# Performance work log

Hardware: AMD Instinct MI355X
Metric: run time of the kernel (lower is better)

The kernel has to match this reference:

```python
import jax, jax.numpy as jnp
import numpy as np

N_HEADS = 16
EPS = 1e-6

def _feature_map(x):
    return jax.nn.elu(x) + 1.0

def setup_inputs() -> dict:
    key = jax.random.key(0)
    k1, k2, k3 = jax.random.split(key, 3)
    B, S, D = 1, 2048, 1024
    x = jax.random.normal(k1, (B, S, D), dtype=jnp.float32)
    causal_mask = jnp.tril(jnp.ones((S, S), dtype=bool))[None, None]  # (1,1,S,S)
    # scale weights like nn.Linear default init (roughly 1/sqrt(fan_in))
    W_qkv = jax.random.normal(k2, (D, 3 * D), dtype=jnp.float32) / np.sqrt(D)
    W_out = jax.random.normal(k3, (D, D), dtype=jnp.float32) / np.sqrt(D)
    return {"x": x, "causal_mask": causal_mask, "W_qkv": W_qkv, "W_out": W_out}

def reference(x, causal_mask, W_qkv, W_out):
    B, S, D = x.shape
    H = N_HEADS
    hd = D // H
    qkv = x @ W_qkv                              # (B,S,3D)
    q, k, v = jnp.split(qkv, 3, axis=-1)
    def to_heads(t):
        return t.reshape(B, S, H, hd).transpose(0, 2, 1, 3)  # (B,H,S,hd)
    q, k, v = to_heads(q), to_heads(k), to_heads(v)
    phi_q = _feature_map(q)
    phi_k = _feature_map(k)
    k_cum = jnp.cumsum(phi_k, axis=2)                        # (B,H,S,hd)
    kv = jnp.einsum('bhsi,bhsj->bhsij', phi_k, v)            # (B,H,S,hd,hd)
    kv_cum = jnp.cumsum(kv, axis=2)
    numer = jnp.einsum('bhsi,bhsij->bhsj', phi_q, kv_cum)    # (B,H,S,hd)
    denom = jnp.einsum('bhsi,bhsi->bhs', phi_q, k_cum) + EPS
    attn_out = numer / denom[..., None]
    attn_out = attn_out.transpose(0, 2, 1, 3).reshape(B, S, D)
    return attn_out @ W_out
```

## Files before the change

kernel.cpp:

```cpp
#include <hip/hip_runtime.h>
#include <cstddef>
#include <cstdint>

#define SEQ 2048
#define DIM 1024
#define NH 16
#define HD 64
#define CK 64
#define NCK (SEQ / CK)
#define KVR 65
#define KVRP 80

typedef __attribute__((ext_vector_type(8))) short short8;
typedef __attribute__((ext_vector_type(8))) unsigned short ushort8;
typedef __attribute__((ext_vector_type(4))) float fx4;

__device__ __forceinline__ float phi_fn(float x) {
    return x > 0.f ? x + 1.f : __expf(x);
}
__device__ __forceinline__ float bf2f(unsigned short u) {
    return __uint_as_float((unsigned int)u << 16);
}
__device__ __forceinline__ unsigned short f2bf(float f) {
    unsigned int u = __float_as_uint(f);
    unsigned int r = (u + 0x7FFFu + ((u >> 16) & 1u)) >> 16;
    return (unsigned short)r;
}

__device__ __forceinline__ short8 lds_read_frag(const unsigned short* base, int row, int kcol) {
    int byte = row * 128 + kcol * 2; byte ^= (row & 7) << 4;
    return *(const short8*)((const char*)base + byte);
}

__device__ __forceinline__ int swz_t(int row, int col) {
    int byte = row * 128 + col * 2;
    return byte ^ ((((row & 7) ^ ((row >> 3) & 7))) << 4);
}
__device__ __forceinline__ void lds_write16_t(unsigned short* base, int row, int col, short8 v) {
    *(short8*)((char*)base + swz_t(row, col)) = v;
}
__device__ __forceinline__ void lds_write2_t(unsigned short* base, int row, int col, unsigned short v) {
    *(unsigned short*)((char*)base + swz_t(row, col)) = v;
}
__device__ __forceinline__ short8 lds_read_frag_t(const unsigned short* base, int row, int kcol) {
    return *(const short8*)((const char*)base + swz_t(row, kcol));
}

template<int N> __device__ __forceinline__ void waitv() {
    if constexpr (N == 0)       asm volatile("s_waitcnt vmcnt(0)"  ::: "memory");
    else if constexpr (N == 4)  asm volatile("s_waitcnt vmcnt(4)"  ::: "memory");
    else if constexpr (N == 5)  asm volatile("s_waitcnt vmcnt(5)"  ::: "memory");
    else if constexpr (N == 6)  asm volatile("s_waitcnt vmcnt(6)"  ::: "memory");
    else if constexpr (N == 8)  asm volatile("s_waitcnt vmcnt(8)"  ::: "memory");
    else if constexpr (N == 10) asm volatile("s_waitcnt vmcnt(10)" ::: "memory");
    else if constexpr (N == 12) asm volatile("s_waitcnt vmcnt(12)" ::: "memory");
    else                        asm volatile("s_waitcnt vmcnt(0)"  ::: "memory");
}

__global__ __launch_bounds__(256)
void prep_fused(const float* __restrict__ x, unsigned short* __restrict__ xb,
                const float* __restrict__ W1, unsigned short* __restrict__ WT1,
                const float* __restrict__ W2, unsigned short* __restrict__ WT2)
{
    __shared__ float t[32][33];
    int b = blockIdx.x;
    if (b < 2048) {
        const int i = (b * 256 + threadIdx.x) * 4;
        float4 v = *(const float4*)&x[i];
        ushort4 o;
        o.x = f2bf(v.x); o.y = f2bf(v.y); o.z = f2bf(v.z); o.w = f2bf(v.w);
        *(ushort4*)&xb[i] = o;
        return;
    }
    b -= 2048;
    const float* W; unsigned short* WT; int N, kb, nb;
    if (b < 96 * 32) {
        W = W1; WT = WT1; N = 3 * DIM;
        nb = (b % 96) * 32; kb = (b / 96) * 32;
    } else {
        b -= 96 * 32;
        W = W2; WT = WT2; N = DIM;
        nb = (b % 32) * 32; kb = (b / 32) * 32;
    }
    const int c = threadIdx.x & 31, r0 = threadIdx.x >> 5;
    #pragma unroll
    for (int i = 0; i < 4; ++i) {
        const int r = r0 + i * 8;
        t[r][c] = W[(size_t)(kb + r) * N + nb + c];
    }
    __syncthreads();
    #pragma unroll
    for (int i = 0; i < 4; ++i) {
        const int r = r0 + i * 8;
        WT[(size_t)(nb + r) * DIM + kb + c] = f2bf(t[c][r]);
    }
}

template<int WAVES_M, int WAVES_N, int NFRAG, int OUT_BF16>
__global__ __launch_bounds__(WAVES_M * WAVES_N * 64)
void gemm_pipe(const unsigned short* __restrict__ A,
               const unsigned short* __restrict__ BT,
               void* __restrict__ Cout, int M, int N, int K)
{
    constexpr int BN      = WAVES_N * NFRAG * 16;
    constexpr int THREADS = WAVES_M * WAVES_N * 64;
    constexpr int CHUNK   = THREADS * 16;
    constexpr int ALOADS  = (128 * 64 * 2) / CHUNK;
    constexpr int BLOADS  = (BN * 64 * 2) / CHUNK;
    constexpr int LOADS   = ALOADS + BLOADS;

    __shared__ unsigned short As[3][128 * 64];
    __shared__ unsigned short Bs[3][BN * 64];

    const int tid = threadIdx.x, lane = tid & 63, wave = tid >> 6;
    const int wm = (wave / WAVES_N) * 64;
    const int wn = (wave % WAVES_N) * (NFRAG * 16);

    int wg = blockIdx.y * gridDim.x + blockIdx.x;
    const int cpx = (gridDim.x * gridDim.y) >> 3;
    wg = (wg & 7) * cpx + (wg >> 3);
    const int bx = wg / gridDim.y;
    const int by = wg % gridDim.y;

    const int m0 = by * 128, n0 = bx * BN;
    const unsigned short* Abase = A + (size_t)m0 * K;
    const unsigned short* Bbase = BT + (size_t)n0 * K;
    const int nt = K >> 6;
    const int fr = lane & 15, fk = (lane >> 4) * 8;

    fx4 acc[4][NFRAG] = {};

    auto STAGE = [&](int slot, int t) {
        const int k0 = t << 6;
        #pragma unroll
        for (int q = 0; q < ALOADS; ++q) {
            const int L = q * CHUNK + tid * 16;
            const int row = L >> 7;
            const int srcb = L ^ ((row & 7) << 4);
            const unsigned short* g = Abase + (size_t)row * K + k0 + ((srcb & 127) >> 1);
            __builtin_amdgcn_global_load_lds(
                (const __attribute__((address_space(1))) void*)g,
                (__attribute__((address_space(3))) void*)((char*)&As[slot][0] + q * CHUNK + wave * 1024),
                16, 0, 0);
        }
        #pragma unroll
        for (int q = 0; q < BLOADS; ++q) {
            const int L = q * CHUNK + tid * 16;
            const int row = L >> 7;
            const int srcb = L ^ ((row & 7) << 4);
            const unsigned short* g = Bbase + (size_t)row * K + k0 + ((srcb & 127) >> 1);
            __builtin_amdgcn_global_load_lds(
                (const __attribute__((address_space(1))) void*)g,
                (__attribute__((address_space(3))) void*)((char*)&Bs[slot][0] + q * CHUNK + wave * 1024),
                16, 0, 0);
        }
    };

    STAGE(0, 0); STAGE(1, 1);
    waitv<LOADS>();
    __builtin_amdgcn_s_barrier();

    for (int t = 0; t < nt; ++t) {
        const int cur = t % 3;
        short8 a0[4], a1[4], b0[NFRAG], b1[NFRAG];
        #pragma unroll
        for (int i = 0; i < 4; ++i) {
            a0[i] = lds_read_frag(&As[cur][0], wm + i * 16 + fr, fk);
            a1[i] = lds_read_frag(&As[cur][0], wm + i * 16 + fr, 32 + fk);
        }
        #pragma unroll
        for (int j = 0; j < NFRAG; ++j) {
            b0[j] = lds_read_frag(&Bs[cur][0], wn + j * 16 + fr, fk);
            b1[j] = lds_read_frag(&Bs[cur][0], wn + j * 16 + fr, 32 + fk);
        }

        const bool pf = (t + 2 < nt);
        if (pf) STAGE((t + 2) % 3, t + 2);

        __builtin_amdgcn_s_setprio(1);
        #pragma unroll
        for (int i = 0; i < 4; ++i)
            #pragma unroll
            for (int j = 0; j < NFRAG; ++j)
                acc[i][j] = __builtin_amdgcn_mfma_f32_16x16x32_bf16(a0[i], b0[j], acc[i][j], 0, 0, 0);
        #pragma unroll
        for (int i = 0; i < 4; ++i)
            #pragma unroll
            for (int j = 0; j < NFRAG; ++j)
                acc[i][j] = __builtin_amdgcn_mfma_f32_16x16x32_bf16(a1[i], b1[j], acc[i][j], 0, 0, 0);
        __builtin_amdgcn_s_setprio(0);

        if (pf) waitv<LOADS>(); else waitv<0>();
        __builtin_amdgcn_s_barrier();
    }

    const int cr = (lane >> 4) * 4, cc = lane & 15;
    #pragma unroll
    for (int i = 0; i < 4; ++i)
        #pragma unroll
        for (int j = 0; j < NFRAG; ++j) {
            const int m = m0 + wm + i * 16 + cr;
            const int n = n0 + wn + j * 16 + cc;
            #pragma unroll
            for (int r = 0; r < 4; ++r) {
                const float v = acc[i][j][r];
                if (OUT_BF16)
                    ((unsigned short*)Cout)[(size_t)(m + r) * N + n] = f2bf(v);
                else
                    ((float*)Cout)[(size_t)(m + r) * N + n] = v;
            }
        }
}

__global__ __launch_bounds__(256)
void chunk_kv(const unsigned short* __restrict__ qkv, float* __restrict__ kvs)
{
    const int c = blockIdx.x, h = blockIdx.y;
    __shared__ unsigned short kT[64 * 64];
    __shared__ unsigned short vT[KVRP * 64];
    const int tid = threadIdx.x, lane = tid & 63, wave = tid >> 6;
    const int s0 = c * CK;

    #pragma unroll
    for (int part = 0; part < 2; ++part) {
        const int s = (tid >> 3) + part * 32;
        const int d0 = (tid & 7) * 8;
        const size_t base = (size_t)(s0 + s) * (3 * DIM) + (size_t)h * HD + d0;
        ushort8 kk = *(const ushort8*)&qkv[base + DIM];
        ushort8 vv = *(const ushort8*)&qkv[base + 2 * DIM];
        #pragma unroll
        for (int u = 0; u < 8; ++u) {
            lds_write2_t(kT, d0 + u, s, f2bf(phi_fn(bf2f(kk[u]))));
            lds_write2_t(vT, d0 + u, s, vv[u]);
        }
    }
    if (tid < 64) lds_write2_t(vT, 64, tid, 0x3F80);
    for (int idx = tid; idx < 15 * 64; idx += 256)
        lds_write2_t(vT, 65 + (idx >> 6), idx & 63, 0);
    __syncthreads();

    fx4 acc[5] = {};
    #pragma unroll
    for (int ks = 0; ks < 2; ++ks) {
        short8 b = lds_read_frag_t(kT, wave * 16 + (lane & 15), ks * 32 + (lane >> 4) * 8);
        #pragma unroll
        for (int mt = 0; mt < 5; ++mt) {
            short8 a = lds_read_frag_t(vT, mt * 16 + (lane & 15), ks * 32 + (lane >> 4) * 8);
            acc[mt] = __builtin_amdgcn_mfma_f32_16x16x32_bf16(a, b, acc[mt], 0, 0, 0);
        }
    }
    float* dst = kvs + (size_t)(h * NCK + c) * KVR * 64;
    const int i = wave * 16 + (lane & 15);
    #pragma unroll
    for (int mt = 0; mt < 5; ++mt)
        #pragma unroll
        for (int t = 0; t < 4; ++t) {
            const int j = mt * 16 + (lane >> 4) * 4 + t;
            if (j < KVR) dst[(size_t)j * 64 + i] = acc[mt][t];
        }
}

__global__ __launch_bounds__(256)
void scan_kv(const float* __restrict__ kvs, unsigned short* __restrict__ kvpb)
{
    const int e = blockIdx.x * 256 + threadIdx.x;
    if (e >= NH * KVR * 64) return;
    const int h = e / (KVR * 64), off = e % (KVR * 64);
    const float* src = kvs + (size_t)h * NCK * KVR * 64 + off;
    unsigned short* dst = kvpb + (size_t)h * NCK * KVR * 64 + off;
    float v[NCK];
    #pragma unroll
    for (int c2 = 0; c2 < NCK; ++c2) v[c2] = src[(size_t)c2 * KVR * 64];
    float run = 0.f;
    #pragma unroll
    for (int c2 = 0; c2 < NCK; ++c2) {
        dst[(size_t)c2 * KVR * 64] = f2bf(run);
        run += v[c2];
    }
}

__global__ __launch_bounds__(256)
void attn_chunk(const unsigned short* __restrict__ qkv,
                const unsigned short* __restrict__ kvpb,
                unsigned short* __restrict__ attnb)
{
    const int c = blockIdx.x, h = blockIdx.y;
    __shared__ unsigned short q_s[64 * 64];
    __shared__ unsigned short k_s[64 * 64];
    __shared__ unsigned short p_s[64 * 64];
    __shared__ unsigned short vT[KVRP * 64];
    __shared__ unsigned short kvp[KVRP * 64];
    const int tid = threadIdx.x, lane = tid & 63, wave = tid >> 6;
    const int s0 = c * CK;

    #pragma unroll
    for (int part = 0; part < 2; ++part) {
        const int s = (tid >> 3) + part * 32;
        const int d0 = (tid & 7) * 8;
        const size_t base = (size_t)(s0 + s) * (3 * DIM) + (size_t)h * HD + d0;
        ushort8 qq = *(const ushort8*)&qkv[base];
        ushort8 kk = *(const ushort8*)&qkv[base + DIM];
        ushort8 vv = *(const ushort8*)&qkv[base + 2 * DIM];
        short8 qo, ko;
        #pragma unroll
        for (int u = 0; u < 8; ++u) {
            qo[u] = (short)f2bf(phi_fn(bf2f(qq[u])));
            ko[u] = (short)f2bf(phi_fn(bf2f(kk[u])));
        }
        lds_write16_t(q_s, s, d0, qo);
        lds_write16_t(k_s, s, d0, ko);
        #pragma unroll
        for (int u = 0; u < 8; ++u)
            lds_write2_t(vT, d0 + u, s, vv[u]);
    }
    {
        const unsigned short* kv_src = kvpb + (size_t)(h * NCK + c) * KVR * 64;
        for (int idx = tid * 8; idx < KVR * 64; idx += 2048) {
            ushort8 kv8 = *(const ushort8*)&kv_src[idx];
            short8 kv8s;
            #pragma unroll
            for (int u = 0; u < 8; ++u) kv8s[u] = (short)kv8[u];
            lds_write16_t(kvp, idx >> 6, idx & 63, kv8s);
        }
    }
    if (tid < 64) lds_write2_t(vT, 64, tid, 0x3F80);
    for (int idx = tid; idx < 15 * 64; idx += 256) {
        lds_write2_t(vT, 65 + (idx >> 6), idx & 63, 0);
        lds_write2_t(kvp, 65 + (idx >> 6), idx & 63, 0);
    }
    __syncthreads();

    const int r0 = wave * 16;
    fx4 accp[4] = {};
    #pragma unroll
    for (int ks = 0; ks < 2; ++ks) {
        short8 aq = lds_read_frag_t(q_s, r0 + (lane & 15), ks * 32 + (lane >> 4) * 8);
        #pragma unroll
        for (int nt = 0; nt < 4; ++nt) {
            short8 bk = lds_read_frag_t(k_s, nt * 16 + (lane & 15), ks * 32 + (lane >> 4) * 8);
            accp[nt] = __builtin_amdgcn_mfma_f32_16x16x32_bf16(aq, bk, accp[nt], 0, 0, 0);
        }
    }
    #pragma unroll
    for (int nt = 0; nt < 4; ++nt)
        #pragma unroll
        for (int t = 0; t < 4; ++t) {
            const int r = r0 + (lane >> 4) * 4 + t, sc = nt * 16 + (lane & 15);
            lds_write2_t(p_s, r, sc, (sc <= r) ? f2bf(accp[nt][t]) : (unsigned short)0);
        }
    __syncthreads();

    fx4 acc[5] = {};
    #pragma unroll
    for (int ks = 0; ks < 2; ++ks) {
        short8 ap = lds_read_frag_t(p_s, r0 + (lane & 15), ks * 32 + (lane >> 4) * 8);
        short8 aq = lds_read_frag_t(q_s, r0 + (lane & 15), ks * 32 + (lane >> 4) * 8);
        #pragma unroll
        for (int nt = 0; nt < 5; ++nt) {
            short8 bv  = lds_read_frag_t(vT,  nt * 16 + (lane & 15), ks * 32 + (lane >> 4) * 8);
            short8 bkv = lds_read_frag_t(kvp, nt * 16 + (lane & 15), ks * 32 + (lane >> 4) * 8);
            acc[nt] = __builtin_amdgcn_mfma_f32_16x16x32_bf16(ap, bv,  acc[nt], 0, 0, 0);
            acc[nt] = __builtin_amdgcn_mfma_f32_16x16x32_bf16(aq, bkv, acc[nt], 0, 0, 0);
        }
    }
    float dinv[4];
    #pragma unroll
    for (int t = 0; t < 4; ++t) {
        const float d = __shfl(acc[4][t], lane & 48, 64);
        dinv[t] = 1.f / (d + 1e-6f);
    }
    #pragma unroll
    for (int nt = 0; nt < 4; ++nt)
        #pragma unroll
        for (int t = 0; t < 4; ++t) {
            const int r = r0 + (lane >> 4) * 4 + t, j = nt * 16 + (lane & 15);
            attnb[(size_t)(s0 + r) * DIM + (size_t)h * HD + j] = f2bf(acc[nt][t] * dinv[t]);
        }
}

extern "C" void kernel_launch(void* const* d_in, const int* in_sizes, int n_in,
                              void* d_out, int out_size, void* d_ws, size_t ws_size,
                              hipStream_t stream)
{
    const float* x     = (const float*)d_in[0];
    const float* W_qkv = (const float*)d_in[2];
    const float* W_out = (const float*)d_in[3];
    float* out = (float*)d_out;

    char* ws = (char*)d_ws;
    size_t off = 0;
    unsigned short* qkvb = (unsigned short*)(ws + off); off += (size_t)SEQ * 3 * DIM * 2;
    unsigned short* xb   = (unsigned short*)(ws + off); off += (size_t)SEQ * DIM * 2;
    float*          kvs  = (float*)         (ws + off); off += (size_t)NH * NCK * KVR * 64 * 4;
    unsigned short* kvpb = (unsigned short*)(ws + off); off += (size_t)NH * NCK * KVR * 64 * 2;
    unsigned short* wqt  = (unsigned short*)(ws + off); off += (size_t)3 * DIM * DIM * 2;
    unsigned short* wot  = (unsigned short*)(ws + off); off += (size_t)DIM * DIM * 2;
    unsigned short* attnb = xb;

    dim3 blk(256);

    prep_fused<<<dim3(2048 + 96 * 32 + 32 * 32), blk, 0, stream>>>(
        x, xb, W_qkv, wqt, W_out, wot);

    gemm_pipe<2, 4, 3, 1><<<dim3(3 * DIM / 192, SEQ / 128), dim3(512), 0, stream>>>(
        xb, wqt, qkvb, SEQ, 3 * DIM, DIM);

    chunk_kv<<<dim3(NCK, NH), blk, 0, stream>>>(qkvb, kvs);
    scan_kv<<<dim3((NH * KVR * 64 + 255) / 256), blk, 0, stream>>>(kvs, kvpb);
    attn_chunk<<<dim3(NCK, NH), blk, 0, stream>>>(qkvb, kvpb, attnb);

    gemm_pipe<2, 2, 2, 0><<<dim3(DIM / 64, SEQ / 128), dim3(256), 0, stream>>>(
        attnb, wot, out, SEQ, DIM, DIM);
}
```

Before: 58.20 us.

## Fuse ELU+1 feature map into QKV GEMM epilogue and reshape GEMM wave layouts

Applies the phi feature map to the Q and K columns inside the QKV GEMM epilogue, so chunk_kv and attn_chunk load already-transformed bf16 values with no per-element conversion. It also changes both GEMM launches to use fewer waves with more fragments per wave (512→256 and 256→128 threads). The epilogue fusion removes duplicated phi work on K across two kernels. The wave reshaping raises register pressure per wave and lowers thread count per block, which may reduce latency hiding.

```diff
diff --git a/kernel.cpp b/kernel.cpp
--- a/kernel.cpp
+++ b/kernel.cpp
@@ -36,8 +36,8 @@
     int byte = row * 128 + col * 2;
     return byte ^ ((((row & 7) ^ ((row >> 3) & 7))) << 4);
 }
-__device__ __forceinline__ void lds_write16_t(unsigned short* base, int row, int col, short8 v) {
-    *(short8*)((char*)base + swz_t(row, col)) = v;
+__device__ __forceinline__ void lds_write16_t(unsigned short* base, int row, int col, ushort8 v) {
+    *(ushort8*)((char*)base + swz_t(row, col)) = v;
 }
 __device__ __forceinline__ void lds_write2_t(unsigned short* base, int row, int col, unsigned short v) {
     *(unsigned short*)((char*)base + swz_t(row, col)) = v;
@@ -96,7 +96,7 @@
     }
 }
 
-template<int WAVES_M, int WAVES_N, int NFRAG, int OUT_BF16>
+template<int WAVES_M, int WAVES_N, int NFRAG, int OUT_BF16, int PHI>
 __global__ __launch_bounds__(WAVES_M * WAVES_N * 64)
 void gemm_pipe(const unsigned short* __restrict__ A,
                const unsigned short* __restrict__ BT,
@@ -203,7 +203,8 @@
             const int n = n0 + wn + j * 16 + cc;
             #pragma unroll
             for (int r = 0; r < 4; ++r) {
-                const float v = acc[i][j][r];
+                float v = acc[i][j][r];
+                if (PHI && n < 2 * DIM) v = phi_fn(v);
                 if (OUT_BF16)
                     ((unsigned short*)Cout)[(size_t)(m + r) * N + n] = f2bf(v);
                 else
@@ -230,7 +231,7 @@
         ushort8 vv = *(const ushort8*)&qkv[base + 2 * DIM];
         #pragma unroll
         for (int u = 0; u < 8; ++u) {
-            lds_write2_t(kT, d0 + u, s, f2bf(phi_fn(bf2f(kk[u]))));
+            lds_write2_t(kT, d0 + u, s, kk[u]);
             lds_write2_t(vT, d0 + u, s, vv[u]);
         }
     }
@@ -301,14 +302,8 @@
         ushort8 qq = *(const ushort8*)&qkv[base];
         ushort8 kk = *(const ushort8*)&qkv[base + DIM];
         ushort8 vv = *(const ushort8*)&qkv[base + 2 * DIM];
-        short8 qo, ko;
-        #pragma unroll
-        for (int u = 0; u < 8; ++u) {
-            qo[u] = (short)f2bf(phi_fn(bf2f(qq[u])));
-            ko[u] = (short)f2bf(phi_fn(bf2f(kk[u])));
-        }
-        lds_write16_t(q_s, s, d0, qo);
-        lds_write16_t(k_s, s, d0, ko);
+        lds_write16_t(q_s, s, d0, qq);
+        lds_write16_t(k_s, s, d0, kk);
         #pragma unroll
         for (int u = 0; u < 8; ++u)
             lds_write2_t(vT, d0 + u, s, vv[u]);
@@ -317,10 +312,7 @@
         const unsigned short* kv_src = kvpb + (size_t)(h * NCK + c) * KVR * 64;
         for (int idx = tid * 8; idx < KVR * 64; idx += 2048) {
             ushort8 kv8 = *(const ushort8*)&kv_src[idx];
-            short8 kv8s;
-            #pragma unroll
-            for (int u = 0; u < 8; ++u) kv8s[u] = (short)kv8[u];
-            lds_write16_t(kvp, idx >> 6, idx & 63, kv8s);
+            lds_write16_t(kvp, idx >> 6, idx & 63, kv8);
         }
     }
     if (tid < 64) lds_write2_t(vT, 64, tid, 0x3F80);
@@ -402,13 +394,13 @@
     prep_fused<<<dim3(2048 + 96 * 32 + 32 * 32), blk, 0, stream>>>(
         x, xb, W_qkv, wqt, W_out, wot);
 
-    gemm_pipe<2, 4, 3, 1><<<dim3(3 * DIM / 192, SEQ / 128), dim3(512), 0, stream>>>(
+    gemm_pipe<2, 2, 6, 1, 1><<<dim3(3 * DIM / 192, SEQ / 128), dim3(256), 0, stream>>>(
         xb, wqt, qkvb, SEQ, 3 * DIM, DIM);
 
     chunk_kv<<<dim3(NCK, NH), blk, 0, stream>>>(qkvb, kvs);
     scan_kv<<<dim3((NH * KVR * 64 + 255) / 256), blk, 0, stream>>>(kvs, kvpb);
     attn_chunk<<<dim3(NCK, NH), blk, 0, stream>>>(qkvb, kvpb, attnb);
 
-    gemm_pipe<2, 2, 2, 0><<<dim3(DIM / 64, SEQ / 128), dim3(256), 0, stream>>>(
+    gemm_pipe<2, 1, 4, 0, 0><<<dim3(DIM / 64, SEQ / 128), dim3(128), 0, stream>>>(
         attnb, wot, out, SEQ, DIM, DIM);
 }
```

Measured after the change: 62.55 us. 7.5% more time.
